# Kernel tuning notes

Hardware: AMD Instinct MI355X
Metric: run time of the kernel (lower is better)

## Reference

```python
import jax, jax.numpy as jnp
import numpy as np

N = 50000
E = 800000
IN_CH = 128
HID = 16
HEADS = 16
OUT_CH = 64
NEG_SLOPE = 0.2
EPS = 1e-16


def _add_self_loops(edge_index, n):
    loops = jnp.arange(n, dtype=edge_index.dtype)
    src = jnp.concatenate([edge_index[0], loops])
    dst = jnp.concatenate([edge_index[1], loops])
    return src, dst


def gat_conv(x, src, dst, W, a_src, a_dst, b, heads, out_ch, concat, n):
    # x: [N, F_in], W: [F_in, heads*out_ch], a_src/a_dst: [heads, out_ch]
    h = (x @ W).reshape(n, heads, out_ch)                 # [N, H, C]
    alpha_src = jnp.sum(h * a_src, axis=-1)               # [N, H]
    alpha_dst = jnp.sum(h * a_dst, axis=-1)               # [N, H]
    e = alpha_src[src] + alpha_dst[dst]                   # [E, H]
    e = jnp.where(e > 0, e, NEG_SLOPE * e)                # LeakyReLU(0.2)
    m = jax.ops.segment_max(e, dst, num_segments=n)       # [N, H] (finite: self-loops)
    ex = jnp.exp(e - m[dst])                              # [E, H]
    denom = jax.ops.segment_sum(ex, dst, num_segments=n)  # [N, H]
    alpha = ex / (denom[dst] + EPS)                       # [E, H]
    msg = h[src] * alpha[:, :, None]                      # [E, H, C]
    out = jax.ops.segment_sum(msg, dst, num_segments=n)   # [N, H, C]
    if concat:
        out = out.reshape(n, heads * out_ch)
    else:
        out = out.mean(axis=1)
    return out + b


def setup_inputs() -> dict:
    key = jax.random.key(0)
    ks = jax.random.split(key, 10)
    x = jax.random.normal(ks[0], (N, IN_CH), dtype=jnp.float32)
    edge_index = jax.random.randint(ks[1], (2, E), 0, N, dtype=jnp.int64)
    s1 = 1.0 / np.sqrt(IN_CH)
    W1 = jax.random.normal(ks[2], (IN_CH, HEADS * HID), dtype=jnp.float32) * s1
    a_src1 = jax.random.normal(ks[3], (HEADS, HID), dtype=jnp.float32) * (1.0 / np.sqrt(HID))
    a_dst1 = jax.random.normal(ks[4], (HEADS, HID), dtype=jnp.float32) * (1.0 / np.sqrt(HID))
    b1 = jnp.zeros((HEADS * HID,), dtype=jnp.float32)
    s2 = 1.0 / np.sqrt(HEADS * HID)
    W2 = jax.random.normal(ks[5], (HEADS * HID, OUT_CH), dtype=jnp.float32) * s2
    a_src2 = jax.random.normal(ks[6], (1, OUT_CH), dtype=jnp.float32) * (1.0 / np.sqrt(OUT_CH))
    a_dst2 = jax.random.normal(ks[7], (1, OUT_CH), dtype=jnp.float32) * (1.0 / np.sqrt(OUT_CH))
    b2 = jnp.zeros((OUT_CH,), dtype=jnp.float32)
    return {"x": x, "edge_index": edge_index, "W1": W1, "a_src1": a_src1,
            "a_dst1": a_dst1, "b1": b1, "W2": W2, "a_src2": a_src2,
            "a_dst2": a_dst2, "b2": b2}


def reference(x, edge_index, W1, a_src1, a_dst1, b1, W2, a_src2, a_dst2, b2):
    src, dst = _add_self_loops(edge_index, N)
    h = gat_conv(x, src, dst, W1, a_src1, a_dst1, b1, HEADS, HID, True, N)
    h = gat_conv(h, src, dst, W2, a_src2, a_dst2, b2, 1, OUT_CH, False, N)
    return jax.nn.sigmoid(h)
```

## Files before the change

kernel.cpp:

```cpp
#include <hip/hip_runtime.h>
#include <hip/hip_bf16.h>

#define NN 50000
#define EE 800000
#define TE 850000
#define BK 64

typedef __hip_bfloat16 bf16;
typedef __attribute__((ext_vector_type(8))) short short8v;
typedef __attribute__((ext_vector_type(4))) float float4v;

__device__ __forceinline__ float b2f(bf16 v) { return __bfloat162float(v); }
__device__ __forceinline__ float bu2f(unsigned short v) {
    return __uint_as_float((unsigned)v << 16);
}
__device__ __forceinline__ unsigned short f2bu(float v) {
    bf16 t = __float2bfloat16(v);
    return *(unsigned short*)&t;
}
__device__ __forceinline__ float lrelu(float e) { return (e > 0.f) ? e : 0.2f * e; }
__device__ __forceinline__ int clampn(int v) {
    return (v < 0) ? 0 : (v >= NN ? NN - 1 : v);
}

__device__ __forceinline__ int block_isi64(const void* ei) {
    __shared__ int sflag;
    int t = threadIdx.x;
    if (t < 64) {
        unsigned z = (((const unsigned*)ei)[2 * t + 1] == 0u) ? 1u : 0u;
        unsigned long long m = __ballot(z);
        if (t == 0) sflag = (__popcll(m) >= 32) ? 1 : 0;
    }
    __syncthreads();
    return sflag;
}

__global__ void prep_k(const void* __restrict__ ei, int* __restrict__ deg,
                       int* __restrict__ csr,
                       const float* __restrict__ W1, const float* __restrict__ W2,
                       const float* __restrict__ asr1, const float* __restrict__ ads1,
                       const float* __restrict__ asr2, const float* __restrict__ ads2,
                       unsigned short* __restrict__ W1T,
                       unsigned short* __restrict__ W2T,
                       unsigned short* __restrict__ P1sT,
                       unsigned short* __restrict__ P1dT,
                       unsigned short* __restrict__ P2T) {
    int isi64 = block_isi64(ei);
    int b = blockIdx.x, t = threadIdx.x;
    if (b < 128) {
        int j = b * 256 + t;
        int n = j >> 7, k = j & 127;
        W1T[j] = f2bu(W1[k * 256 + n]);
    } else if (b < 192) {
        int j = (b - 128) * 256 + t;
        int n = j >> 8, k = j & 255;
        W2T[j] = f2bu(W2[k * 64 + n]);
    } else if (b == 192) {
        for (int j = t; j < 2048; j += 256) {
            int h = j >> 7, k = j & 127;
            float s = 0.f, d = 0.f;
            for (int c = 0; c < 16; ++c) {
                float wv = W1[k * 256 + h * 16 + c];
                s += wv * asr1[h * 16 + c];
                d += wv * ads1[h * 16 + c];
            }
            P1sT[j] = f2bu(s);
            P1dT[j] = f2bu(d);
        }
    } else if (b == 193) {
        int k = t;
        float s = 0.f, d = 0.f;
        for (int c = 0; c < 64; ++c) {
            float wv = W2[k * 64 + c];
            s += wv * asr2[c];
            d += wv * ads2[c];
        }
        P2T[k] = f2bu(s);
        P2T[256 + k] = f2bu(d);
        for (int j = 512 + t; j < 4096; j += 256) P2T[j] = 0;
    }
    int p = b * 256 + t;
    int i0 = p * 2;
    if (i0 >= TE) return;
    int s0, d0, s1 = -1, d1 = -1;
    if (i0 + 1 < EE) {
        if (isi64) {
            longlong2 sv = ((const longlong2*)ei)[p];
            longlong2 dv = ((const longlong2*)ei)[(EE >> 1) + p];
            s0 = clampn((int)sv.x); s1 = clampn((int)sv.y);
            d0 = clampn((int)dv.x); d1 = clampn((int)dv.y);
        } else {
            int2 sv = ((const int2*)ei)[p];
            int2 dv = ((const int2*)ei)[(EE >> 1) + p];
            s0 = clampn(sv.x); s1 = clampn(sv.y);
            d0 = clampn(dv.x); d1 = clampn(dv.y);
        }
    } else {
        auto lde = [&](long long idx) {
            return clampn(isi64 ? (int)((const long long*)ei)[idx] : ((const int*)ei)[idx]);
        };
        if (i0 < EE) { s0 = lde(i0); d0 = lde((long long)EE + i0); }
        else         { s0 = i0 - EE; d0 = i0 - EE; }
        if (i0 + 1 < TE) {
            if (i0 + 1 < EE) { s1 = lde(i0 + 1); d1 = lde((long long)EE + i0 + 1); }
            else             { s1 = i0 + 1 - EE; d1 = i0 + 1 - EE; }
        }
    }
    int pos0 = atomicAdd(&deg[d0], 1);
    if (pos0 < BK) csr[d0 * BK + pos0] = s0;
    if (d1 >= 0) {
        int pos1 = atomicAdd(&deg[d1], 1);
        if (pos1 < BK) csr[d1 * BK + pos1] = s1;
    }
}

__global__ __launch_bounds__(256) void gemm1_k(
    const float* __restrict__ x, const unsigned short* __restrict__ W1T,
    const unsigned short* __restrict__ P1sT, const unsigned short* __restrict__ P1dT,
    bf16* __restrict__ h1, float* __restrict__ a_src, float* __restrict__ a_dst) {
    int wv = threadIdx.x >> 6, lane = threadIdx.x & 63;
    int m = lane & 15, quad = lane >> 4;
    int row0 = blockIdx.x * 64 + wv * 16;
    int arow = row0 + m;
    int arowc = (arow < NN) ? arow : NN - 1;
    const float4* x4 = (const float4*)x;
    short8v a[4];
#pragma unroll
    for (int ks = 0; ks < 4; ++ks) {
        float4 f0 = x4[(size_t)arowc * 32 + ks * 8 + quad * 2];
        float4 f1 = x4[(size_t)arowc * 32 + ks * 8 + quad * 2 + 1];
        union { short8v v; unsigned short u[8]; } ua;
        ua.u[0] = f2bu(f0.x); ua.u[1] = f2bu(f0.y);
        ua.u[2] = f2bu(f0.z); ua.u[3] = f2bu(f0.w);
        ua.u[4] = f2bu(f1.x); ua.u[5] = f2bu(f1.y);
        ua.u[6] = f2bu(f1.z); ua.u[7] = f2bu(f1.w);
        a[ks] = ua.v;
    }
    float4v accs = {0.f, 0.f, 0.f, 0.f}, accd = {0.f, 0.f, 0.f, 0.f};
#pragma unroll
    for (int ks = 0; ks < 4; ++ks) {
        short8v bs = *(const short8v*)&P1sT[(size_t)m * 128 + quad * 8 + ks * 32];
        short8v bd = *(const short8v*)&P1dT[(size_t)m * 128 + quad * 8 + ks * 32];
        accs = __builtin_amdgcn_mfma_f32_16x16x32_bf16(a[ks], bs, accs, 0, 0, 0);
        accd = __builtin_amdgcn_mfma_f32_16x16x32_bf16(a[ks], bd, accd, 0, 0, 0);
    }
    float4v acc[16];
#pragma unroll
    for (int t = 0; t < 16; ++t) {
        float4v c = {0.f, 0.f, 0.f, 0.f};
        const unsigned short* wb = &W1T[(size_t)(t * 16 + m) * 128 + quad * 8];
#pragma unroll
        for (int ks = 0; ks < 4; ++ks) {
            short8v b = *(const short8v*)&wb[ks * 32];
            c = __builtin_amdgcn_mfma_f32_16x16x32_bf16(a[ks], b, c, 0, 0, 0);
        }
        acc[t] = c;
    }
#pragma unroll
    for (int t = 0; t < 16; ++t) {
#pragma unroll
        for (int r = 0; r < 4; ++r) {
            int orow = row0 + quad * 4 + r;
            if (orow < NN)
                h1[(size_t)orow * 256 + t * 16 + m] = __float2bfloat16(acc[t][r]);
        }
    }
#pragma unroll
    for (int r = 0; r < 4; ++r) {
        int orow = row0 + quad * 4 + r;
        if (orow < NN) {
            a_src[orow * 16 + m] = accs[r];
            a_dst[orow * 16 + m] = accd[r];
        }
    }
}

__global__ __launch_bounds__(256) void agg1_k(
    const int* __restrict__ deg, int* __restrict__ csr,
    const float* __restrict__ a_src, const float* __restrict__ a_dst,
    const bf16* __restrict__ h1, const float* __restrict__ b1,
    bf16* __restrict__ out1) {
    __shared__ int sbuf[4][64];
    int wv = threadIdx.x >> 6, lane = threadIdx.x & 63;
    int dst = blockIdx.x * 4 + wv;
    int d = deg[dst]; if (d > BK) d = BK;
    int base = dst * BK;
    int v = (lane < d) ? csr[base + lane] : 0x7fffffff;
    int rank = 0;
    for (int j = 0; j < d; ++j) {
        int vj = __shfl(v, j, 64);
        rank += (vj < v || (vj == v && j < lane)) ? 1 : 0;
    }
    if (lane < d) sbuf[wv][rank] = v;
    if (lane < d) csr[base + lane] = sbuf[wv][lane];
    int we = lane >> 4, wh = lane & 15;
    int hc = lane >> 2;
    float adst_w = a_dst[dst * 16 + wh];
    float ax = 0.f, ay = 0.f, az = 0.f, aw = 0.f;
    float dsum = 0.f;
    int t0 = 0;
    for (; t0 + 4 <= d; t0 += 4) {
        int sr = sbuf[wv][t0 + we];
        float wr = __expf(lrelu(a_src[sr * 16 + wh] + adst_w));
        dsum += wr;
#pragma unroll
        for (int j = 0; j < 4; ++j) {
            float wj = __shfl(wr, j * 16 + hc, 64);
            int sj = sbuf[wv][t0 + j];
            ushort4 hv = *(const ushort4*)&h1[(size_t)sj * 256 + lane * 4];
            ax += wj * bu2f(hv.x);
            ay += wj * bu2f(hv.y);
            az += wj * bu2f(hv.z);
            aw += wj * bu2f(hv.w);
        }
    }
    if (t0 < d) {
        int n = d - t0;
        float wr = 0.f;
        if (we < n) {
            int sr = sbuf[wv][t0 + we];
            wr = __expf(lrelu(a_src[sr * 16 + wh] + adst_w));
        }
        dsum += wr;
        for (int j = 0; j < n; ++j) {
            float wj = __shfl(wr, j * 16 + hc, 64);
            int sj = sbuf[wv][t0 + j];
            ushort4 hv = *(const ushort4*)&h1[(size_t)sj * 256 + lane * 4];
            ax += wj * bu2f(hv.x);
            ay += wj * bu2f(hv.y);
            az += wj * bu2f(hv.z);
            aw += wj * bu2f(hv.w);
        }
    }
    dsum += __shfl_xor(dsum, 16, 64);
    dsum += __shfl_xor(dsum, 32, 64);
    float invd = 1.f / (__shfl(dsum, hc, 64) + 1e-16f);
    float4 bv = *(const float4*)&b1[lane * 4];
    ushort4 st;
    st.x = f2bu(ax * invd + bv.x);
    st.y = f2bu(ay * invd + bv.y);
    st.z = f2bu(az * invd + bv.z);
    st.w = f2bu(aw * invd + bv.w);
    *(ushort4*)&out1[(size_t)dst * 256 + lane * 4] = st;
}

__global__ __launch_bounds__(256) void gemm2_k(
    const bf16* __restrict__ out1, const unsigned short* __restrict__ W2T,
    const unsigned short* __restrict__ P2T,
    bf16* __restrict__ h2, float* __restrict__ a_src2, float* __restrict__ a_dst2) {
    int wv = threadIdx.x >> 6, lane = threadIdx.x & 63;
    int m = lane & 15, quad = lane >> 4;
    int row0 = blockIdx.x * 64 + wv * 16;
    int arow = row0 + m;
    int arowc = (arow < NN) ? arow : NN - 1;
    const unsigned short* ab = (const unsigned short*)out1;
    short8v a[8];
#pragma unroll
    for (int ks = 0; ks < 8; ++ks)
        a[ks] = *(const short8v*)&ab[(size_t)arowc * 256 + ks * 32 + quad * 8];
    float4v acca = {0.f, 0.f, 0.f, 0.f};
#pragma unroll
    for (int ks = 0; ks < 8; ++ks) {
        short8v b = *(const short8v*)&P2T[(size_t)m * 256 + quad * 8 + ks * 32];
        acca = __builtin_amdgcn_mfma_f32_16x16x32_bf16(a[ks], b, acca, 0, 0, 0);
    }
    float4v acc[4];
#pragma unroll
    for (int t = 0; t < 4; ++t) {
        float4v c = {0.f, 0.f, 0.f, 0.f};
        const unsigned short* wb = &W2T[(size_t)(t * 16 + m) * 256 + quad * 8];
#pragma unroll
        for (int ks = 0; ks < 8; ++ks) {
            short8v b = *(const short8v*)&wb[ks * 32];
            c = __builtin_amdgcn_mfma_f32_16x16x32_bf16(a[ks], b, c, 0, 0, 0);
        }
        acc[t] = c;
    }
#pragma unroll
    for (int t = 0; t < 4; ++t) {
#pragma unroll
        for (int r = 0; r < 4; ++r) {
            int orow = row0 + quad * 4 + r;
            if (orow < NN)
                h2[(size_t)orow * 64 + t * 16 + m] = __float2bfloat16(acc[t][r]);
        }
    }
#pragma unroll
    for (int r = 0; r < 4; ++r) {
        int orow = row0 + quad * 4 + r;
        if (orow < NN) {
            if (m == 0) a_src2[orow] = acca[r];
            if (m == 1) a_dst2[orow] = acca[r];
        }
    }
}

__global__ __launch_bounds__(256) void agg2_k(
    const int* __restrict__ deg, const int* __restrict__ csr,
    const float* __restrict__ a_src2, const float* __restrict__ a_dst2,
    const bf16* __restrict__ h2, const float* __restrict__ b2,
    float* __restrict__ out) {
    int wv = threadIdx.x >> 6;
    int lane = threadIdx.x & 63;
    int dst = blockIdx.x * 4 + wv;
    if (dst >= NN) return;
    int d = deg[dst]; if (d > BK) d = BK;
    int base = dst * BK;
    float adst = a_dst2[dst];
    int half = lane >> 5, hl = lane & 31;
    float acc0 = 0.f, acc1 = 0.f, dsum = 0.f;
    float wr = 0.f; int sr = 0;
    if (lane < d) {
        sr = csr[base + lane];
        wr = __expf(lrelu(a_src2[sr] + adst));
    }
    dsum += wr;
    for (int j0 = 0; j0 < d; j0 += 8) {
        ushort2 hv[4];
        float wj[4];
#pragma unroll
        for (int u = 0; u < 4; ++u) {
            int j = j0 + u * 2 + half;
            int jc = (j < d) ? j : 0;
            float w = __shfl(wr, jc, 64);
            int sj = __shfl(sr, jc, 64);
            wj[u] = (j < d) ? w : 0.f;
            hv[u] = *(const ushort2*)&h2[(size_t)sj * 64 + hl * 2];
        }
#pragma unroll
        for (int u = 0; u < 4; ++u) {
            acc0 += wj[u] * bu2f(hv[u].x);
            acc1 += wj[u] * bu2f(hv[u].y);
        }
    }
    acc0 += __shfl_xor(acc0, 32, 64);
    acc1 += __shfl_xor(acc1, 32, 64);
#pragma unroll
    for (int o = 32; o >= 1; o >>= 1) dsum += __shfl_xor(dsum, o, 64);
    if (half == 0) {
        float inv = 1.f / (dsum + 1e-16f);
        float o0 = acc0 * inv + b2[hl * 2];
        float o1 = acc1 * inv + b2[hl * 2 + 1];
        float2 st;
        st.x = 1.f / (1.f + __expf(-o0));
        st.y = 1.f / (1.f + __expf(-o1));
        *(float2*)&out[(size_t)dst * 64 + hl * 2] = st;
    }
}


extern "C" void kernel_launch(void* const* d_in, const int* in_sizes, int n_in,
                              void* d_out, int out_size, void* d_ws, size_t ws_size,
                              hipStream_t stream) {
    const float* x    = (const float*)d_in[0];
    const void*  ei   = d_in[1];
    const float* W1   = (const float*)d_in[2];
    const float* asr1 = (const float*)d_in[3];
    const float* ads1 = (const float*)d_in[4];
    const float* b1   = (const float*)d_in[5];
    const float* W2   = (const float*)d_in[6];
    const float* asr2 = (const float*)d_in[7];
    const float* ads2 = (const float*)d_in[8];
    const float* b2   = (const float*)d_in[9];
    float* out = (float*)d_out;

    char* w = (char*)d_ws;
    auto carve = [&](size_t bytes) {
        void* p = (void*)w;
        w += (bytes + 255) & ~(size_t)255;
        return p;
    };
    int*    csr      = (int*)carve((size_t)NN * BK * 4);
    int*    deg      = (int*)carve((size_t)NN * 4);
    float*  a_src1   = (float*)carve((size_t)NN * 16 * 4);
    float*  a_dst1   = (float*)carve((size_t)NN * 16 * 4);
    unsigned short* W1T  = (unsigned short*)carve(128 * 256 * 2);
    unsigned short* W2T  = (unsigned short*)carve(256 * 64 * 2);
    unsigned short* P1sT = (unsigned short*)carve(16 * 128 * 2);
    unsigned short* P1dT = (unsigned short*)carve(16 * 128 * 2);
    unsigned short* P2T  = (unsigned short*)carve(16 * 256 * 2);
    bf16*   h1       = (bf16*)carve((size_t)NN * 256 * 2);
    bf16*   out1     = (bf16*)carve((size_t)NN * 256 * 2);
    char*   l2base   = (char*)h1;
    bf16*   h2       = (bf16*)l2base;
    float*  a_src2   = (float*)(l2base + (size_t)NN * 64 * 2);
    float*  a_dst2   = a_src2 + NN;

    hipMemsetAsync(deg, 0, (size_t)NN * 4, stream);

    const int pgrid = ((TE + 1) / 2 + 255) / 256;
    prep_k<<<pgrid, 256, 0, stream>>>(ei, deg, csr, W1, W2, asr1, ads1, asr2, ads2,
                                      W1T, W2T, P1sT, P1dT, P2T);
    gemm1_k<<<(NN + 63) / 64, 256, 0, stream>>>(x, W1T, P1sT, P1dT, h1, a_src1, a_dst1);
    agg1_k<<<NN / 4, 256, 0, stream>>>(deg, csr, a_src1, a_dst1, h1, b1, out1);
    gemm2_k<<<(NN + 63) / 64, 256, 0, stream>>>(out1, W2T, P2T, h2, a_src2, a_dst2);
    agg2_k<<<(NN + 3) / 4, 256, 0, stream>>>(deg, csr, a_src2, a_dst2, h2, b2, out);
}
```

Before: 299.3 us.

## Fuse edge CSR build with layer-1 GEMM into one launch, drop memset

The degree memset is folded into a small weight-prep kernel. The edge-bucketing pass and the first GEMM are merged into one kernel whose block range is split between GEMM tiles and edge-scatter blocks. The aim is to overlap the atomic-heavy CSR build with the MFMA GEMM and to remove one launch plus the memset. The cost is an extra, smaller prep launch and a heterogeneous kernel with mixed register and LDS demands.

```diff
diff --git a/kernel.cpp b/kernel.cpp
--- a/kernel.cpp
+++ b/kernel.cpp
@@ -5,12 +5,13 @@
 #define EE 800000
 #define TE 850000
 #define BK 64
+#define NGB 782
+#define NEB 1661
 
 typedef __hip_bfloat16 bf16;
 typedef __attribute__((ext_vector_type(8))) short short8v;
 typedef __attribute__((ext_vector_type(4))) float float4v;
 
-__device__ __forceinline__ float b2f(bf16 v) { return __bfloat162float(v); }
 __device__ __forceinline__ float bu2f(unsigned short v) {
     return __uint_as_float((unsigned)v << 16);
 }
@@ -23,30 +24,15 @@
     return (v < 0) ? 0 : (v >= NN ? NN - 1 : v);
 }
 
-__device__ __forceinline__ int block_isi64(const void* ei) {
-    __shared__ int sflag;
-    int t = threadIdx.x;
-    if (t < 64) {
-        unsigned z = (((const unsigned*)ei)[2 * t + 1] == 0u) ? 1u : 0u;
-        unsigned long long m = __ballot(z);
-        if (t == 0) sflag = (__popcll(m) >= 32) ? 1 : 0;
-    }
-    __syncthreads();
-    return sflag;
-}
-
-__global__ void prep_k(const void* __restrict__ ei, int* __restrict__ deg,
-                       int* __restrict__ csr,
-                       const float* __restrict__ W1, const float* __restrict__ W2,
-                       const float* __restrict__ asr1, const float* __restrict__ ads1,
-                       const float* __restrict__ asr2, const float* __restrict__ ads2,
-                       unsigned short* __restrict__ W1T,
-                       unsigned short* __restrict__ W2T,
-                       unsigned short* __restrict__ P1sT,
-                       unsigned short* __restrict__ P1dT,
-                       unsigned short* __restrict__ P2T) {
-    int isi64 = block_isi64(ei);
+__global__ __launch_bounds__(256) void wprep_k(
+    const float* __restrict__ W1, const float* __restrict__ W2,
+    const float* __restrict__ asr1, const float* __restrict__ ads1,
+    const float* __restrict__ asr2, const float* __restrict__ ads2,
+    unsigned short* __restrict__ W1T, unsigned short* __restrict__ W2T,
+    unsigned short* __restrict__ P1sT, unsigned short* __restrict__ P1dT,
+    unsigned short* __restrict__ P2T, int* __restrict__ deg) {
     int b = blockIdx.x, t = threadIdx.x;
+    for (int i = b * 256 + t; i < NN; i += 256 * 256) deg[i] = 0;
     if (b < 128) {
         int j = b * 256 + t;
         int n = j >> 7, k = j & 127;
@@ -79,7 +65,82 @@
         P2T[256 + k] = f2bu(d);
         for (int j = 512 + t; j < 4096; j += 256) P2T[j] = 0;
     }
-    int p = b * 256 + t;
+}
+
+__global__ __launch_bounds__(256) void eg1_k(
+    const void* __restrict__ ei, const float* __restrict__ x,
+    const unsigned short* __restrict__ W1T,
+    const unsigned short* __restrict__ P1sT, const unsigned short* __restrict__ P1dT,
+    int* __restrict__ deg, int* __restrict__ csr,
+    bf16* __restrict__ h1, float* __restrict__ a_src, float* __restrict__ a_dst) {
+    if (blockIdx.x < NGB) {
+        int wv = threadIdx.x >> 6, lane = threadIdx.x & 63;
+        int m = lane & 15, quad = lane >> 4;
+        int row0 = blockIdx.x * 64 + wv * 16;
+        int arow = row0 + m;
+        int arowc = (arow < NN) ? arow : NN - 1;
+        const float4* x4 = (const float4*)x;
+        short8v a[4];
+#pragma unroll
+        for (int ks = 0; ks < 4; ++ks) {
+            float4 f0 = x4[(size_t)arowc * 32 + ks * 8 + quad * 2];
+            float4 f1 = x4[(size_t)arowc * 32 + ks * 8 + quad * 2 + 1];
+            union { short8v v; unsigned short u[8]; } ua;
+            ua.u[0] = f2bu(f0.x); ua.u[1] = f2bu(f0.y);
+            ua.u[2] = f2bu(f0.z); ua.u[3] = f2bu(f0.w);
+            ua.u[4] = f2bu(f1.x); ua.u[5] = f2bu(f1.y);
+            ua.u[6] = f2bu(f1.z); ua.u[7] = f2bu(f1.w);
+            a[ks] = ua.v;
+        }
+        float4v accs = {0.f, 0.f, 0.f, 0.f}, accd = {0.f, 0.f, 0.f, 0.f};
+#pragma unroll
+        for (int ks = 0; ks < 4; ++ks) {
+            short8v bs = *(const short8v*)&P1sT[(size_t)m * 128 + quad * 8 + ks * 32];
+            short8v bd = *(const short8v*)&P1dT[(size_t)m * 128 + quad * 8 + ks * 32];
+            accs = __builtin_amdgcn_mfma_f32_16x16x32_bf16(a[ks], bs, accs, 0, 0, 0);
+            accd = __builtin_amdgcn_mfma_f32_16x16x32_bf16(a[ks], bd, accd, 0, 0, 0);
+        }
+        float4v acc[16];
+#pragma unroll
+        for (int t = 0; t < 16; ++t) {
+            float4v c = {0.f, 0.f, 0.f, 0.f};
+            const unsigned short* wb = &W1T[(size_t)(t * 16 + m) * 128 + quad * 8];
+#pragma unroll
+            for (int ks = 0; ks < 4; ++ks) {
+                short8v b = *(const short8v*)&wb[ks * 32];
+                c = __builtin_amdgcn_mfma_f32_16x16x32_bf16(a[ks], b, c, 0, 0, 0);
+            }
+            acc[t] = c;
+        }
+#pragma unroll
+        for (int t = 0; t < 16; ++t) {
+#pragma unroll
+            for (int r = 0; r < 4; ++r) {
+                int orow = row0 + quad * 4 + r;
+                if (orow < NN)
+                    h1[(size_t)orow * 256 + t * 16 + m] = __float2bfloat16(acc[t][r]);
+            }
+        }
+#pragma unroll
+        for (int r = 0; r < 4; ++r) {
+            int orow = row0 + quad * 4 + r;
+            if (orow < NN) {
+                a_src[orow * 16 + m] = accs[r];
+                a_dst[orow * 16 + m] = accd[r];
+            }
+        }
+        return;
+    }
+    __shared__ int sflag;
+    int t = threadIdx.x;
+    if (t < 64) {
+        unsigned z = (((const unsigned*)ei)[2 * t + 1] == 0u) ? 1u : 0u;
+        unsigned long long mb = __ballot(z);
+        if (t == 0) sflag = (__popcll(mb) >= 32) ? 1 : 0;
+    }
+    __syncthreads();
+    int isi64 = sflag;
+    int p = (blockIdx.x - NGB) * 256 + t;
     int i0 = p * 2;
     if (i0 >= TE) return;
     int s0, d0, s1 = -1, d1 = -1;
@@ -111,67 +172,6 @@
     if (d1 >= 0) {
         int pos1 = atomicAdd(&deg[d1], 1);
         if (pos1 < BK) csr[d1 * BK + pos1] = s1;
-    }
-}
-
-__global__ __launch_bounds__(256) void gemm1_k(
-    const float* __restrict__ x, const unsigned short* __restrict__ W1T,
-    const unsigned short* __restrict__ P1sT, const unsigned short* __restrict__ P1dT,
-    bf16* __restrict__ h1, float* __restrict__ a_src, float* __restrict__ a_dst) {
-    int wv = threadIdx.x >> 6, lane = threadIdx.x & 63;
-    int m = lane & 15, quad = lane >> 4;
-    int row0 = blockIdx.x * 64 + wv * 16;
-    int arow = row0 + m;
-    int arowc = (arow < NN) ? arow : NN - 1;
-    const float4* x4 = (const float4*)x;
-    short8v a[4];
-#pragma unroll
-    for (int ks = 0; ks < 4; ++ks) {
-        float4 f0 = x4[(size_t)arowc * 32 + ks * 8 + quad * 2];
-        float4 f1 = x4[(size_t)arowc * 32 + ks * 8 + quad * 2 + 1];
-        union { short8v v; unsigned short u[8]; } ua;
-        ua.u[0] = f2bu(f0.x); ua.u[1] = f2bu(f0.y);
-        ua.u[2] = f2bu(f0.z); ua.u[3] = f2bu(f0.w);
-        ua.u[4] = f2bu(f1.x); ua.u[5] = f2bu(f1.y);
-        ua.u[6] = f2bu(f1.z); ua.u[7] = f2bu(f1.w);
-        a[ks] = ua.v;
-    }
-    float4v accs = {0.f, 0.f, 0.f, 0.f}, accd = {0.f, 0.f, 0.f, 0.f};
-#pragma unroll
-    for (int ks = 0; ks < 4; ++ks) {
-        short8v bs = *(const short8v*)&P1sT[(size_t)m * 128 + quad * 8 + ks * 32];
-        short8v bd = *(const short8v*)&P1dT[(size_t)m * 128 + quad * 8 + ks * 32];
-        accs = __builtin_amdgcn_mfma_f32_16x16x32_bf16(a[ks], bs, accs, 0, 0, 0);
-        accd = __builtin_amdgcn_mfma_f32_16x16x32_bf16(a[ks], bd, accd, 0, 0, 0);
-    }
-    float4v acc[16];
-#pragma unroll
-    for (int t = 0; t < 16; ++t) {
-        float4v c = {0.f, 0.f, 0.f, 0.f};
-        const unsigned short* wb = &W1T[(size_t)(t * 16 + m) * 128 + quad * 8];
-#pragma unroll
-        for (int ks = 0; ks < 4; ++ks) {
-            short8v b = *(const short8v*)&wb[ks * 32];
-            c = __builtin_amdgcn_mfma_f32_16x16x32_bf16(a[ks], b, c, 0, 0, 0);
-        }
-        acc[t] = c;
-    }
-#pragma unroll
-    for (int t = 0; t < 16; ++t) {
-#pragma unroll
-        for (int r = 0; r < 4; ++r) {
-            int orow = row0 + quad * 4 + r;
-            if (orow < NN)
-                h1[(size_t)orow * 256 + t * 16 + m] = __float2bfloat16(acc[t][r]);
-        }
-    }
-#pragma unroll
-    for (int r = 0; r < 4; ++r) {
-        int orow = row0 + quad * 4 + r;
-        if (orow < NN) {
-            a_src[orow * 16 + m] = accs[r];
-            a_dst[orow * 16 + m] = accd[r];
-        }
     }
 }
 
@@ -386,12 +386,10 @@
     float*  a_src2   = (float*)(l2base + (size_t)NN * 64 * 2);
     float*  a_dst2   = a_src2 + NN;
 
-    hipMemsetAsync(deg, 0, (size_t)NN * 4, stream);
-
-    const int pgrid = ((TE + 1) / 2 + 255) / 256;
-    prep_k<<<pgrid, 256, 0, stream>>>(ei, deg, csr, W1, W2, asr1, ads1, asr2, ads2,
-                                      W1T, W2T, P1sT, P1dT, P2T);
-    gemm1_k<<<(NN + 63) / 64, 256, 0, stream>>>(x, W1T, P1sT, P1dT, h1, a_src1, a_dst1);
+    wprep_k<<<256, 256, 0, stream>>>(W1, W2, asr1, ads1, asr2, ads2,
+                                     W1T, W2T, P1sT, P1dT, P2T, deg);
+    eg1_k<<<NGB + NEB, 256, 0, stream>>>(ei, x, W1T, P1sT, P1dT,
+                                         deg, csr, h1, a_src1, a_dst1);
     agg1_k<<<NN / 4, 256, 0, stream>>>(deg, csr, a_src1, a_dst1, h1, b1, out1);
     gemm2_k<<<(NN + 63) / 64, 256, 0, stream>>>(out1, W2T, P2T, h2, a_src2, a_dst2);
     agg2_k<<<(NN + 3) / 4, 256, 0, stream>>>(deg, csr, a_src2, a_dst2, h2, b2, out);
```

Result: faster. 270.9 us (-9.5%).
